# Kernel tuning notes

Hardware: AMD Instinct MI355X
Metric: run time of the kernel (lower is better)

## Reference

```python
import jax, jax.numpy as jnp
import numpy as np

N_NODES = 10000
N_EDGES = 160000
HIDDEN = 64
NUM_RBF = 32
Q_DIM = 8
CUTOFF_UPPER = 5.0


def silu(x):
    return x * jax.nn.sigmoid(x)


def tensor_norm(X):
    # X: [n, 3, 3, H] -> [n, H] (Frobenius norm squared over the 3x3 dims)
    return (X * X).sum(axis=(1, 2))


def decompose_tensor(X):
    # X: [n, 3, 3, H] -> I: [n, H] (trace/3), A: antisym [n,3,3,H], S: sym traceless [n,3,3,H]
    eye = jnp.eye(3, dtype=X.dtype)[None, :, :, None]
    I = jnp.einsum('naah->nh', X) / 3.0
    Xt = X.transpose(0, 2, 1, 3)
    A = 0.5 * (X - Xt)
    S = 0.5 * (X + Xt) - I[:, None, None, :] * eye
    return I, A, S


def compose_tensor(I, A, S):
    eye = jnp.eye(3, dtype=A.dtype)[None, :, :, None]
    return I[:, None, None, :] * eye + A + S


def tmm(P, Q):
    # 3x3 matmul per (atom, channel): [n,3,3,H] x [n,3,3,H] -> [n,3,3,H]
    return jnp.einsum('nach,ncbh->nabh', P, Q)


def setup_inputs() -> dict:
    key = jax.random.key(0)
    ks = jax.random.split(key, 16)
    H = HIDDEN
    inp = {
        'X': jax.random.normal(ks[0], (N_NODES, 3, 3, H), jnp.float32),
        'charges': jax.random.normal(ks[1], (N_NODES, Q_DIM), jnp.float32),
        'edge_weight': jax.random.uniform(ks[2], (N_EDGES,), jnp.float32) * CUTOFF_UPPER,
        'edge_attr': jax.random.normal(ks[3], (N_EDGES, NUM_RBF), jnp.float32),
        'edge_index': jax.random.randint(ks[4], (2, N_EDGES), 0, N_NODES, jnp.int32),
    }
    d_in = NUM_RBF + 2 * Q_DIM
    inp['Ws1'] = jax.random.normal(ks[5], (d_in, H), jnp.float32) / np.sqrt(d_in).astype(np.float32)
    inp['bs1'] = jnp.zeros((H,), jnp.float32)
    inp['Ws2'] = jax.random.normal(ks[6], (H, 2 * H), jnp.float32) / np.sqrt(H).astype(np.float32)
    inp['bs2'] = jnp.zeros((2 * H,), jnp.float32)
    inp['Ws3'] = jax.random.normal(ks[7], (2 * H, 3 * H), jnp.float32) / np.sqrt(2 * H).astype(np.float32)
    inp['bs3'] = jnp.zeros((3 * H,), jnp.float32)
    for i in range(6):
        inp['Wt%d' % i] = jax.random.normal(ks[8 + i], (H, H), jnp.float32) / np.sqrt(H).astype(np.float32)
    return inp


def reference(X, charges, edge_weight, edge_attr, Ws1, bs1, Ws2, bs2, Ws3, bs3,
              Wt0, Wt1, Wt2, Wt3, Wt4, Wt5, edge_index):
    H = HIDDEN
    n = X.shape[0]
    row, col = edge_index[0], edge_index[1]
    # cosine cutoff (cutoff_lower = 0)
    C = 0.5 * (jnp.cos(edge_weight * (jnp.pi / CUTOFF_UPPER)) + 1.0)
    C = C * (edge_weight < CUTOFF_UPPER).astype(X.dtype)
    # edge scalar MLP on [rbf, q_i, q_j]
    h = jnp.concatenate([edge_attr, charges[row], charges[col]], axis=-1)
    h = silu(h @ Ws1 + bs1)
    h = silu(h @ Ws2 + bs2)
    h = silu(h @ Ws3 + bs3)
    w = (h * C[:, None]).reshape(h.shape[0], 3, H)  # [E, 3, H]
    # normalize node tensors
    X = X / (tensor_norm(X) + 1.0)[:, None, None, :]
    I, A, S = decompose_tensor(X)
    I = I @ Wt0
    A = A @ Wt1
    S = S @ Wt2
    Y = compose_tensor(I, A, S)
    # message passing: gather I/A/S at source (edge_index[1]), weight per component, scatter-add at dest (edge_index[0])
    eye = jnp.eye(3, dtype=X.dtype)[None, :, :, None]
    msg_e = ((w[:, 0] * I[col])[:, None, None, :] * eye
             + w[:, 1][:, None, None, :] * A[col]
             + w[:, 2][:, None, None, :] * S[col])  # [E, 3, 3, H]
    msg = jax.ops.segment_sum(msg_e, row, num_segments=n)  # [n, 3, 3, H]
    # O(3): C = msg @ Y + Y @ msg (3x3 matmul per channel)
    Cm = tmm(msg, Y) + tmm(Y, msg)
    I2, A2, S2 = decompose_tensor(Cm)
    normp1 = tensor_norm(Cm) + 1.0
    I2 = I2 / normp1
    A2 = A2 / normp1[:, None, None, :]
    S2 = S2 / normp1[:, None, None, :]
    I2 = I2 @ Wt3
    A2 = A2 @ Wt4
    S2 = S2 @ Wt5
    dX = compose_tensor(I2, A2, S2)
    return X + dX + tmm(dX, dX)
```

## Files before the change

### kernel.cpp

```cpp
#include <hip/hip_runtime.h>
#include <math.h>

#define HD 64

typedef _Float16 half8 __attribute__((ext_vector_type(8)));
typedef _Float16 half4v __attribute__((ext_vector_type(4)));
typedef float floatx4 __attribute__((ext_vector_type(4)));

__device__ __forceinline__ float silu_f(float x) {
    return x * __builtin_amdgcn_rcpf(1.0f + __expf(-x));
}

__global__ __launch_bounds__(256) void node_pre(
    const float* __restrict__ X,
    const float* __restrict__ Wt0, const float* __restrict__ Wt1, const float* __restrict__ Wt2,
    float* __restrict__ Tn, _Float16* __restrict__ TnH, int N)
{
    int sub = threadIdx.x >> 6;
    int h = threadIdx.x & 63;
    int n = blockIdx.x * 4 + sub;
    int nn = (n < N) ? n : (N - 1);

    const float* Xb = X + (size_t)nn * 9 * HD + h;
    float x[9];
    float nrm = 0.f;
#pragma unroll
    for (int i = 0; i < 9; ++i) { x[i] = Xb[i * HD]; nrm += x[i] * x[i]; }
    float inv = 1.0f / (nrm + 1.0f);
#pragma unroll
    for (int i = 0; i < 9; ++i) x[i] *= inv;

    float I0 = (x[0] + x[4] + x[8]) * (1.0f / 3.0f);
    __shared__ float comp[4][10][HD];
    comp[sub][0][h] = I0;
    comp[sub][1][h] = 0.5f * (x[1] - x[3]);
    comp[sub][2][h] = 0.5f * (x[2] - x[6]);
    comp[sub][3][h] = 0.5f * (x[5] - x[7]);
    comp[sub][4][h] = x[0] - I0;
    comp[sub][5][h] = 0.5f * (x[1] + x[3]);
    comp[sub][6][h] = 0.5f * (x[2] + x[6]);
    comp[sub][7][h] = x[4] - I0;
    comp[sub][8][h] = 0.5f * (x[5] + x[7]);
    comp[sub][9][h] = x[8] - I0;
    __syncthreads();
    float acc[10];
#pragma unroll
    for (int i = 0; i < 10; ++i) acc[i] = 0.f;
    for (int k = 0; k < HD; ++k) {
        float w0 = Wt0[k * HD + h];
        float w1 = Wt1[k * HD + h];
        float w2 = Wt2[k * HD + h];
        acc[0] += comp[sub][0][k] * w0;
        acc[1] += comp[sub][1][k] * w1;
        acc[2] += comp[sub][2][k] * w1;
        acc[3] += comp[sub][3][k] * w1;
#pragma unroll
        for (int j = 0; j < 6; ++j) acc[4 + j] += comp[sub][4 + j][k] * w2;
    }
    if (n < N) {
        float* tp = Tn + (size_t)n * 640 + h;
        _Float16* th = TnH + (size_t)n * 640 + h;
#pragma unroll
        for (int i = 0; i < 10; ++i) {
            tp[i * 64] = acc[i];
            th[i * 64] = (_Float16)acc[i];
        }
    }
}

__global__ __launch_bounds__(256) void count_kernel(
    const int* __restrict__ edge_index, int* __restrict__ cnt, int E)
{
    int e = blockIdx.x * 256 + threadIdx.x;
    if (e < E) atomicAdd(&cnt[edge_index[e]], 1);
}

__global__ __launch_bounds__(1024) void scanA(
    const int* __restrict__ cnt, int* __restrict__ offs, int* __restrict__ partial, int N)
{
    __shared__ int wsum[16];
    int tid = threadIdx.x, wid = tid >> 6, lane = tid & 63;
    int i = blockIdx.x * 1024 + tid;
    int v = (i < N) ? cnt[i] : 0;
    int s = v;
#pragma unroll
    for (int d = 1; d < 64; d <<= 1) {
        int t = __shfl_up(s, d, 64);
        if (lane >= d) s += t;
    }
    if (lane == 63) wsum[wid] = s;
    __syncthreads();
    if (tid == 0) {
        int run = 0;
#pragma unroll
        for (int w = 0; w < 16; ++w) { int t = wsum[w]; wsum[w] = run; run += t; }
        partial[blockIdx.x] = run;
    }
    __syncthreads();
    if (i < N) offs[i] = wsum[wid] + s - v;
}

__global__ __launch_bounds__(64) void scanB(int* __restrict__ partial, int nb)
{
    int lane = threadIdx.x;
    int v = (lane < nb) ? partial[lane] : 0;
    int s = v;
#pragma unroll
    for (int d = 1; d < 64; d <<= 1) {
        int t = __shfl_up(s, d, 64);
        if (lane >= d) s += t;
    }
    if (lane < nb) partial[lane] = s - v;
}

__global__ __launch_bounds__(256) void scanC(
    int* __restrict__ offs, const int* __restrict__ partial, int* __restrict__ curs,
    int N, int E)
{
    int i = blockIdx.x * 256 + threadIdx.x;
    if (i < N) {
        int o = offs[i] + partial[i >> 10];
        offs[i] = o;
        curs[i] = o;
    }
    if (i == 0) offs[N] = E;
}

__global__ __launch_bounds__(256) void place_kernel(
    const int* __restrict__ edge_index, int* __restrict__ curs,
    int* __restrict__ rank, int* __restrict__ colP, int E)
{
    int e = blockIdx.x * 256 + threadIdx.x;
    if (e < E) {
        int p = atomicAdd(&curs[edge_index[e]], 1);
        rank[e] = p;
        colP[p] = edge_index[E + e];
    }
}

__global__ __launch_bounds__(256) void wconv(
    const float* __restrict__ Ws1, const float* __restrict__ Ws2, const float* __restrict__ Ws3,
    _Float16* __restrict__ W1f, _Float16* __restrict__ W2f, _Float16* __restrict__ W3f)
{
    int id = blockIdx.x * 256 + threadIdx.x;
    if (id < 4096) {
        int i = id & 7, l = (id >> 3) & 63, t = id >> 9;
        int s = t >> 2, nt = t & 3;
        int k = s * 32 + (l >> 4) * 8 + i;
        int n = nt * 16 + (l & 15);
        W1f[id] = (k < 48) ? (_Float16)Ws1[k * 64 + n] : (_Float16)0.f;
    } else if (id < 4096 + 8192) {
        int j = id - 4096;
        int i = j & 7, l = (j >> 3) & 63, t = j >> 9;
        int s = t >> 3, nt = t & 7;
        int k = s * 32 + (l >> 4) * 8 + i;
        int n = nt * 16 + (l & 15);
        W2f[j] = (_Float16)Ws2[k * 128 + n];
    } else if (id < 4096 + 8192 + 24576) {
        int j = id - 4096 - 8192;
        int i = j & 7, l = (j >> 3) & 63, t = j >> 9;
        int s = t / 12, nt = t % 12;
        int k = s * 32 + (l >> 4) * 8 + i;
        int n = nt * 16 + (l & 15);
        W3f[j] = (_Float16)Ws3[k * 192 + n];
    }
}

__global__ __launch_bounds__(256, 4) void mlp_mfma(
    const float* __restrict__ edge_attr, const float* __restrict__ charges,
    const float* __restrict__ edge_weight, const int* __restrict__ edge_index,
    const int* __restrict__ rank,
    const _Float16* __restrict__ W1f, const float* __restrict__ bs1,
    const _Float16* __restrict__ W2f, const float* __restrict__ bs2,
    const _Float16* __restrict__ W3f, const float* __restrict__ bs3,
    _Float16* __restrict__ bufH, int E)
{
    __shared__ __align__(16) _Float16 act[4][16][200];
    __shared__ float cvsS[4][16];
    __shared__ int rankSS[4][16];

    int tid = threadIdx.x;
    int wv = tid >> 6, l = tid & 63;
    int base = blockIdx.x * 64 + wv * 16;
    int row16 = l & 15, quad = l >> 4;

#pragma unroll
    for (int i = 0; i < 4; ++i) {
        int slot = l + i * 64;
        int e_l = slot >> 4, f = slot & 15;
        int e = base + e_l;
        int ee = (e < E) ? e : (E - 1);
        float4 v = make_float4(0.f, 0.f, 0.f, 0.f);
        if (f < 8) {
            v = *(const float4*)(edge_attr + (size_t)ee * 32 + f * 4);
        } else if (f < 10) {
            int r = edge_index[ee];
            v = *(const float4*)(charges + (size_t)r * 8 + (f - 8) * 4);
        } else if (f < 12) {
            int c = edge_index[E + ee];
            v = *(const float4*)(charges + (size_t)c * 8 + (f - 10) * 4);
        }
        half4v hv = { (_Float16)v.x, (_Float16)v.y, (_Float16)v.z, (_Float16)v.w };
        *(half4v*)&act[wv][e_l][f * 4] = hv;
    }
    if (l < 16) {
        int e = base + l;
        int ee = (e < E) ? e : (E - 1);
        rankSS[wv][l] = rank[ee];
        float wgt = edge_weight[ee];
        float cv = 0.5f * (__cosf(wgt * 0.6283185307179586f) + 1.0f);
        cvsS[wv][l] = (wgt < 5.0f) ? cv : 0.0f;
    }

    half8 A[4];
    A[0] = *(const half8*)&act[wv][row16][quad * 8];
    A[1] = *(const half8*)&act[wv][row16][32 + quad * 8];
    floatx4 acc1[4];
    {
        half8 W[8];
#pragma unroll
        for (int t = 0; t < 8; ++t)
            W[t] = *(const half8*)(W1f + ((size_t)t * 64 + l) * 8);
#pragma unroll
        for (int nt = 0; nt < 4; ++nt) {
            floatx4 c = {0.f, 0.f, 0.f, 0.f};
            c = __builtin_amdgcn_mfma_f32_16x16x32_f16(A[0], W[nt], c, 0, 0, 0);
            c = __builtin_amdgcn_mfma_f32_16x16x32_f16(A[1], W[4 + nt], c, 0, 0, 0);
            acc1[nt] = c;
        }
    }
#pragma unroll
    for (int nt = 0; nt < 4; ++nt) {
        float b = bs1[nt * 16 + row16];
#pragma unroll
        for (int r = 0; r < 4; ++r)
            act[wv][quad * 4 + r][64 + nt * 16 + row16] = (_Float16)silu_f(acc1[nt][r] + b);
    }

    A[0] = *(const half8*)&act[wv][row16][64 + quad * 8];
    A[1] = *(const half8*)&act[wv][row16][96 + quad * 8];
    floatx4 acc2[8];
#pragma unroll
    for (int nt = 0; nt < 8; ++nt) acc2[nt] = (floatx4){0.f, 0.f, 0.f, 0.f};
#pragma unroll
    for (int s = 0; s < 2; ++s) {
        half8 W[8];
#pragma unroll
        for (int nt = 0; nt < 8; ++nt)
            W[nt] = *(const half8*)(W2f + ((size_t)(s * 8 + nt) * 64 + l) * 8);
#pragma unroll
        for (int nt = 0; nt < 8; ++nt)
            acc2[nt] = __builtin_amdgcn_mfma_f32_16x16x32_f16(A[s], W[nt], acc2[nt], 0, 0, 0);
    }
#pragma unroll
    for (int nt = 0; nt < 8; ++nt) {
        float b = bs2[nt * 16 + row16];
#pragma unroll
        for (int r = 0; r < 4; ++r)
            act[wv][quad * 4 + r][nt * 16 + row16] = (_Float16)silu_f(acc2[nt][r] + b);
    }

    A[0] = *(const half8*)&act[wv][row16][quad * 8];
    A[1] = *(const half8*)&act[wv][row16][32 + quad * 8];
    A[2] = *(const half8*)&act[wv][row16][64 + quad * 8];
    A[3] = *(const half8*)&act[wv][row16][96 + quad * 8];

    float cvrow[4];
#pragma unroll
    for (int r = 0; r < 4; ++r) cvrow[r] = cvsS[wv][quad * 4 + r];

#pragma unroll
    for (int g = 0; g < 2; ++g) {
        floatx4 acc3[6];
#pragma unroll
        for (int j = 0; j < 6; ++j) acc3[j] = (floatx4){0.f, 0.f, 0.f, 0.f};
#pragma unroll
        for (int s = 0; s < 4; ++s) {
            half8 W[6];
#pragma unroll
            for (int j = 0; j < 6; ++j)
                W[j] = *(const half8*)(W3f + ((size_t)(s * 12 + g * 6 + j) * 64 + l) * 8);
#pragma unroll
            for (int j = 0; j < 6; ++j)
                acc3[j] = __builtin_amdgcn_mfma_f32_16x16x32_f16(A[s], W[j], acc3[j], 0, 0, 0);
        }
#pragma unroll
        for (int j = 0; j < 6; ++j) {
            int nt = g * 6 + j;
            float b = bs3[nt * 16 + row16];
#pragma unroll
            for (int r = 0; r < 4; ++r)
                act[wv][quad * 4 + r][nt * 16 + row16] =
                    (_Float16)(silu_f(acc3[j][r] + b) * cvrow[r]);
        }
    }
    {
        int fr = l >> 2;
        int ef = base + fr;
        if (ef < E) {
            _Float16* dst = bufH + (size_t)rankSS[wv][fr] * 192;
#pragma unroll
            for (int i = 0; i < 6; ++i) {
                int j = (l & 3) + i * 4;
                *(half8*)(dst + j * 8) = *(const half8*)&act[wv][fr][j * 8];
            }
        }
    }
}

__global__ __launch_bounds__(256) void msg_kernel(
    const _Float16* __restrict__ bufH, const int* __restrict__ colP,
    const int* __restrict__ offs, const _Float16* __restrict__ TnH,
    float* __restrict__ Mn, int N)
{
    __shared__ float part[2][2][10][64];
    int slot = threadIdx.x >> 7;
    int half = (threadIdx.x >> 6) & 1;
    int lane = threadIdx.x & 63;
    int n = blockIdx.x * 2 + slot;
    int nn = (n < N) ? n : (N - 1);
    int beg = offs[nn], end = offs[nn + 1];
    int mid = beg + ((end - beg + 1) >> 1);
    int s0 = half ? mid : beg;
    int s1 = half ? end : mid;

    float a0 = 0.f, a1 = 0.f, a2 = 0.f, a3 = 0.f, a4 = 0.f;
    float a5 = 0.f, a6 = 0.f, a7 = 0.f, a8 = 0.f, a9 = 0.f;
#pragma unroll 2
    for (int idx = s0; idx < s1; ++idx) {
        int c = colP[idx];
        const _Float16* wp = bufH + (size_t)idx * 192;
        float w0 = (float)wp[lane];
        float w1 = (float)wp[64 + lane];
        float w2 = (float)wp[128 + lane];
        const _Float16* tp = TnH + (size_t)c * 640;
        a0 += w0 * (float)tp[lane];
        a1 += w1 * (float)tp[64 + lane];
        a2 += w1 * (float)tp[128 + lane];
        a3 += w1 * (float)tp[192 + lane];
        a4 += w2 * (float)tp[256 + lane];
        a5 += w2 * (float)tp[320 + lane];
        a6 += w2 * (float)tp[384 + lane];
        a7 += w2 * (float)tp[448 + lane];
        a8 += w2 * (float)tp[512 + lane];
        a9 += w2 * (float)tp[576 + lane];
    }
    part[slot][half][0][lane] = a0; part[slot][half][1][lane] = a1;
    part[slot][half][2][lane] = a2; part[slot][half][3][lane] = a3;
    part[slot][half][4][lane] = a4; part[slot][half][5][lane] = a5;
    part[slot][half][6][lane] = a6; part[slot][half][7][lane] = a7;
    part[slot][half][8][lane] = a8; part[slot][half][9][lane] = a9;
    __syncthreads();

    if (n < N) {
        float* mp = Mn + (size_t)n * 640;
#pragma unroll
        for (int j = 0; j < 5; ++j) {
            int c = half * 5 + j;
            mp[c * 64 + lane] = part[slot][0][c][lane] + part[slot][1][c][lane];
        }
    }
}

__global__ __launch_bounds__(256) void node_post(
    const float* __restrict__ X,
    const float* __restrict__ Tn, const float* __restrict__ Mn,
    const float* __restrict__ Wt3, const float* __restrict__ Wt4, const float* __restrict__ Wt5,
    float* __restrict__ out, int N)
{
    int sub = threadIdx.x >> 6;
    int h = threadIdx.x & 63;
    int n = blockIdx.x * 4 + sub;
    int nn = (n < N) ? n : (N - 1);

    const float* Xb = X + (size_t)nn * 9 * HD + h;
    float x[9];
    float nr = 0.f;
#pragma unroll
    for (int i = 0; i < 9; ++i) { x[i] = Xb[i * HD]; nr += x[i] * x[i]; }
    float xinv = 1.0f / (nr + 1.0f);
#pragma unroll
    for (int i = 0; i < 9; ++i) x[i] *= xinv;

    const float* tp = Tn + (size_t)nn * 640 + h;
    const float* mp = Mn + (size_t)nn * 640 + h;
    float yI = tp[0], mI = mp[0];
    float yA[3], yS[6], mA[3], mS[6];
#pragma unroll
    for (int j = 0; j < 3; ++j) { yA[j] = tp[(1 + j) * 64]; mA[j] = mp[(1 + j) * 64]; }
#pragma unroll
    for (int j = 0; j < 6; ++j) { yS[j] = tp[(4 + j) * 64]; mS[j] = mp[(4 + j) * 64]; }

    float M[3][3] = {
        { mI + mS[0],     mA[0] + mS[1],   mA[1] + mS[2] },
        { -mA[0] + mS[1], mI + mS[3],      mA[2] + mS[4] },
        { -mA[1] + mS[2], -mA[2] + mS[4],  mI + mS[5] } };
    float Y[3][3] = {
        { yI + yS[0],     yA[0] + yS[1],   yA[1] + yS[2] },
        { -yA[0] + yS[1], yI + yS[3],      yA[2] + yS[4] },
        { -yA[1] + yS[2], -yA[2] + yS[4],  yI + yS[5] } };

    float Cm[3][3];
    float nrm = 0.f;
#pragma unroll
    for (int a = 0; a < 3; ++a) {
#pragma unroll
        for (int b = 0; b < 3; ++b) {
            float s = 0.f;
#pragma unroll
            for (int c = 0; c < 3; ++c) s += M[a][c] * Y[c][b] + Y[a][c] * M[c][b];
            Cm[a][b] = s;
            nrm += s * s;
        }
    }
    float inv = 1.0f / (nrm + 1.0f);
    float tr3 = (Cm[0][0] + Cm[1][1] + Cm[2][2]) * (1.0f / 3.0f);

    __shared__ float comp[4][10][HD];
    comp[sub][0][h] = tr3 * inv;
    comp[sub][1][h] = 0.5f * (Cm[0][1] - Cm[1][0]) * inv;
    comp[sub][2][h] = 0.5f * (Cm[0][2] - Cm[2][0]) * inv;
    comp[sub][3][h] = 0.5f * (Cm[1][2] - Cm[2][1]) * inv;
    comp[sub][4][h] = (Cm[0][0] - tr3) * inv;
    comp[sub][5][h] = 0.5f * (Cm[0][1] + Cm[1][0]) * inv;
    comp[sub][6][h] = 0.5f * (Cm[0][2] + Cm[2][0]) * inv;
    comp[sub][7][h] = (Cm[1][1] - tr3) * inv;
    comp[sub][8][h] = 0.5f * (Cm[1][2] + Cm[2][1]) * inv;
    comp[sub][9][h] = (Cm[2][2] - tr3) * inv;
    __syncthreads();

    float acc[10];
#pragma unroll
    for (int i = 0; i < 10; ++i) acc[i] = 0.f;
    for (int k = 0; k < HD; ++k) {
        float w3 = Wt3[k * HD + h];
        float w4 = Wt4[k * HD + h];
        float w5 = Wt5[k * HD + h];
        acc[0] += comp[sub][0][k] * w3;
        acc[1] += comp[sub][1][k] * w4;
        acc[2] += comp[sub][2][k] * w4;
        acc[3] += comp[sub][3][k] * w4;
#pragma unroll
        for (int j = 0; j < 6; ++j) acc[4 + j] += comp[sub][4 + j][k] * w5;
    }
    float D[3][3] = {
        { acc[0] + acc[4],  acc[1] + acc[5],  acc[2] + acc[6] },
        { -acc[1] + acc[5], acc[0] + acc[7],  acc[3] + acc[8] },
        { -acc[2] + acc[6], -acc[3] + acc[8], acc[0] + acc[9] } };

    if (n < N) {
        float* ob = out + (size_t)n * 9 * HD + h;
#pragma unroll
        for (int a = 0; a < 3; ++a) {
#pragma unroll
            for (int b = 0; b < 3; ++b) {
                float s = 0.f;
#pragma unroll
                for (int c = 0; c < 3; ++c) s += D[a][c] * D[c][b];
                ob[(a * 3 + b) * HD] = x[a * 3 + b] + D[a][b] + s;
            }
        }
    }
}

extern "C" void kernel_launch(void* const* d_in, const int* in_sizes, int n_in,
                              void* d_out, int out_size, void* d_ws, size_t ws_size,
                              hipStream_t stream)
{
    const float* X           = (const float*)d_in[0];
    const float* charges     = (const float*)d_in[1];
    const float* edge_weight = (const float*)d_in[2];
    const float* edge_attr   = (const float*)d_in[3];
    const int*   edge_index  = (const int*)d_in[4];
    const float* Ws1 = (const float*)d_in[5];
    const float* bs1 = (const float*)d_in[6];
    const float* Ws2 = (const float*)d_in[7];
    const float* bs2 = (const float*)d_in[8];
    const float* Ws3 = (const float*)d_in[9];
    const float* bs3 = (const float*)d_in[10];
    const float* Wt0 = (const float*)d_in[11];
    const float* Wt1 = (const float*)d_in[12];
    const float* Wt2 = (const float*)d_in[13];
    const float* Wt3 = (const float*)d_in[14];
    const float* Wt4 = (const float*)d_in[15];
    const float* Wt5 = (const float*)d_in[16];

    int N = in_sizes[0] / (9 * HD);
    int E = in_sizes[2];

    float* ws = (float*)d_ws;
    float* Tn  = ws;
    float* Mn  = Tn + (size_t)N * 640;
    _Float16* TnH  = (_Float16*)(Mn + (size_t)N * 640);
    _Float16* bufH = TnH + (size_t)N * 640;
    int* cnt   = (int*)(bufH + (size_t)E * 192);
    int* offs  = cnt + N;
    int* curs  = offs + N + 1;
    int* rank  = curs + N;
    int* colP  = rank + E;
    int* partial = colP + E;
    size_t fofs = ((size_t)((char*)(partial + 64) - (char*)d_ws) + 15) & ~(size_t)15;
    _Float16* W1f = (_Float16*)((char*)d_ws + fofs);
    _Float16* W2f = W1f + 4096;
    _Float16* W3f = W2f + 8192;

    hipMemsetAsync(cnt, 0, (size_t)N * sizeof(int), stream);

    int nbE256 = (E + 255) / 256;
    int nbN1024 = (N + 1023) / 1024;
    count_kernel<<<nbE256, 256, 0, stream>>>(edge_index, cnt, E);
    scanA<<<nbN1024, 1024, 0, stream>>>(cnt, offs, partial, N);
    scanB<<<1, 64, 0, stream>>>(partial, nbN1024);
    scanC<<<(N + 255) / 256, 256, 0, stream>>>(offs, partial, curs, N, E);
    place_kernel<<<nbE256, 256, 0, stream>>>(edge_index, curs, rank, colP, E);

    wconv<<<144, 256, 0, stream>>>(Ws1, Ws2, Ws3, W1f, W2f, W3f);

    node_pre<<<(N + 3) / 4, 256, 0, stream>>>(X, Wt0, Wt1, Wt2, Tn, TnH, N);

    int nbE64 = (E + 63) / 64;
    mlp_mfma<<<nbE64, 256, 0, stream>>>(edge_attr, charges, edge_weight, edge_index,
                                        rank, W1f, bs1, W2f, bs2, W3f, bs3, bufH, E);

    msg_kernel<<<(N + 1) / 2, 256, 0, stream>>>(bufH, colP, offs, TnH, Mn, N);

    node_post<<<(N + 3) / 4, 256, 0, stream>>>(X, Tn, Mn, Wt3, Wt4, Wt5, (float*)d_out, N);
}
```

Before: 178.8 us.

## Merge small kernels and give each MLP wave two 16-edge tiles

The weight-conversion kernel is folded into node_pre as extra blocks of one launch, and the single-block scanB is removed by having scanC sum the preceding block partials itself. mlp_mfma now runs 128-thread blocks in which each wave handles 32 edges as two M-tiles, so every loaded weight fragment feeds two MFMAs. This cuts launch count and weight-load traffic per edge. The cost is more accumulator registers per wave and a per-thread serial loop over partials in scanC.

```diff
diff --git a/kernel.cpp b/kernel.cpp
--- a/kernel.cpp
+++ b/kernel.cpp
@@ -11,11 +11,39 @@
     return x * __builtin_amdgcn_rcpf(1.0f + __expf(-x));
 }
 
-__global__ __launch_bounds__(256) void node_pre(
+__global__ __launch_bounds__(256) void pre_wconv(
     const float* __restrict__ X,
     const float* __restrict__ Wt0, const float* __restrict__ Wt1, const float* __restrict__ Wt2,
-    float* __restrict__ Tn, _Float16* __restrict__ TnH, int N)
-{
+    float* __restrict__ Tn, _Float16* __restrict__ TnH, int N, int nbPre,
+    const float* __restrict__ Ws1, const float* __restrict__ Ws2, const float* __restrict__ Ws3,
+    _Float16* __restrict__ W1f, _Float16* __restrict__ W2f, _Float16* __restrict__ W3f)
+{
+    if (blockIdx.x >= nbPre) {
+        int id = (blockIdx.x - nbPre) * 256 + threadIdx.x;
+        if (id < 4096) {
+            int i = id & 7, l = (id >> 3) & 63, t = id >> 9;
+            int s = t >> 2, nt = t & 3;
+            int k = s * 32 + (l >> 4) * 8 + i;
+            int n = nt * 16 + (l & 15);
+            W1f[id] = (k < 48) ? (_Float16)Ws1[k * 64 + n] : (_Float16)0.f;
+        } else if (id < 4096 + 8192) {
+            int j = id - 4096;
+            int i = j & 7, l = (j >> 3) & 63, t = j >> 9;
+            int s = t >> 3, nt = t & 7;
+            int k = s * 32 + (l >> 4) * 8 + i;
+            int n = nt * 16 + (l & 15);
+            W2f[j] = (_Float16)Ws2[k * 128 + n];
+        } else if (id < 4096 + 8192 + 24576) {
+            int j = id - 4096 - 8192;
+            int i = j & 7, l = (j >> 3) & 63, t = j >> 9;
+            int s = t / 12, nt = t % 12;
+            int k = s * 32 + (l >> 4) * 8 + i;
+            int n = nt * 16 + (l & 15);
+            W3f[j] = (_Float16)Ws3[k * 192 + n];
+        }
+        return;
+    }
+
     int sub = threadIdx.x >> 6;
     int h = threadIdx.x & 63;
     int n = blockIdx.x * 4 + sub;
@@ -100,26 +128,16 @@
     if (i < N) offs[i] = wsum[wid] + s - v;
 }
 
-__global__ __launch_bounds__(64) void scanB(int* __restrict__ partial, int nb)
-{
-    int lane = threadIdx.x;
-    int v = (lane < nb) ? partial[lane] : 0;
-    int s = v;
-#pragma unroll
-    for (int d = 1; d < 64; d <<= 1) {
-        int t = __shfl_up(s, d, 64);
-        if (lane >= d) s += t;
-    }
-    if (lane < nb) partial[lane] = s - v;
-}
-
 __global__ __launch_bounds__(256) void scanC(
     int* __restrict__ offs, const int* __restrict__ partial, int* __restrict__ curs,
     int N, int E)
 {
     int i = blockIdx.x * 256 + threadIdx.x;
     if (i < N) {
-        int o = offs[i] + partial[i >> 10];
+        int b = i >> 10;
+        int basev = 0;
+        for (int w = 0; w < b; ++w) basev += partial[w];
+        int o = offs[i] + basev;
         offs[i] = o;
         curs[i] = o;
     }
@@ -138,35 +156,7 @@
     }
 }
 
-__global__ __launch_bounds__(256) void wconv(
-    const float* __restrict__ Ws1, const float* __restrict__ Ws2, const float* __restrict__ Ws3,
-    _Float16* __restrict__ W1f, _Float16* __restrict__ W2f, _Float16* __restrict__ W3f)
-{
-    int id = blockIdx.x * 256 + threadIdx.x;
-    if (id < 4096) {
-        int i = id & 7, l = (id >> 3) & 63, t = id >> 9;
-        int s = t >> 2, nt = t & 3;
-        int k = s * 32 + (l >> 4) * 8 + i;
-        int n = nt * 16 + (l & 15);
-        W1f[id] = (k < 48) ? (_Float16)Ws1[k * 64 + n] : (_Float16)0.f;
-    } else if (id < 4096 + 8192) {
-        int j = id - 4096;
-        int i = j & 7, l = (j >> 3) & 63, t = j >> 9;
-        int s = t >> 3, nt = t & 7;
-        int k = s * 32 + (l >> 4) * 8 + i;
-        int n = nt * 16 + (l & 15);
-        W2f[j] = (_Float16)Ws2[k * 128 + n];
-    } else if (id < 4096 + 8192 + 24576) {
-        int j = id - 4096 - 8192;
-        int i = j & 7, l = (j >> 3) & 63, t = j >> 9;
-        int s = t / 12, nt = t % 12;
-        int k = s * 32 + (l >> 4) * 8 + i;
-        int n = nt * 16 + (l & 15);
-        W3f[j] = (_Float16)Ws3[k * 192 + n];
-    }
-}
-
-__global__ __launch_bounds__(256, 4) void mlp_mfma(
+__global__ __launch_bounds__(128, 4) void mlp_mfma(
     const float* __restrict__ edge_attr, const float* __restrict__ charges,
     const float* __restrict__ edge_weight, const int* __restrict__ edge_index,
     const int* __restrict__ rank,
@@ -175,17 +165,17 @@
     const _Float16* __restrict__ W3f, const float* __restrict__ bs3,
     _Float16* __restrict__ bufH, int E)
 {
-    __shared__ __align__(16) _Float16 act[4][16][200];
-    __shared__ float cvsS[4][16];
-    __shared__ int rankSS[4][16];
+    __shared__ __align__(16) _Float16 act[2][32][200];
+    __shared__ float cvsS[2][32];
+    __shared__ int rankSS[2][32];
 
     int tid = threadIdx.x;
     int wv = tid >> 6, l = tid & 63;
-    int base = blockIdx.x * 64 + wv * 16;
+    int base = blockIdx.x * 64 + wv * 32;
     int row16 = l & 15, quad = l >> 4;
 
 #pragma unroll
-    for (int i = 0; i < 4; ++i) {
+    for (int i = 0; i < 8; ++i) {
         int slot = l + i * 64;
         int e_l = slot >> 4, f = slot & 15;
         int e = base + e_l;
@@ -203,7 +193,7 @@
         half4v hv = { (_Float16)v.x, (_Float16)v.y, (_Float16)v.z, (_Float16)v.w };
         *(half4v*)&act[wv][e_l][f * 4] = hv;
     }
-    if (l < 16) {
+    if (l < 32) {
         int e = base + l;
         int ee = (e < E) ? e : (E - 1);
         rankSS[wv][l] = rank[ee];
@@ -212,90 +202,127 @@
         cvsS[wv][l] = (wgt < 5.0f) ? cv : 0.0f;
     }
 
-    half8 A[4];
-    A[0] = *(const half8*)&act[wv][row16][quad * 8];
-    A[1] = *(const half8*)&act[wv][row16][32 + quad * 8];
-    floatx4 acc1[4];
+    half8 A[2][2];
+#pragma unroll
+    for (int m = 0; m < 2; ++m) {
+        A[m][0] = *(const half8*)&act[wv][m * 16 + row16][quad * 8];
+        A[m][1] = *(const half8*)&act[wv][m * 16 + row16][32 + quad * 8];
+    }
     {
         half8 W[8];
 #pragma unroll
         for (int t = 0; t < 8; ++t)
             W[t] = *(const half8*)(W1f + ((size_t)t * 64 + l) * 8);
+        floatx4 acc[2][4];
+#pragma unroll
+        for (int nt = 0; nt < 4; ++nt)
+#pragma unroll
+            for (int m = 0; m < 2; ++m) {
+                floatx4 c = {0.f, 0.f, 0.f, 0.f};
+                c = __builtin_amdgcn_mfma_f32_16x16x32_f16(A[m][0], W[nt], c, 0, 0, 0);
+                c = __builtin_amdgcn_mfma_f32_16x16x32_f16(A[m][1], W[4 + nt], c, 0, 0, 0);
+                acc[m][nt] = c;
+            }
 #pragma unroll
         for (int nt = 0; nt < 4; ++nt) {
-            floatx4 c = {0.f, 0.f, 0.f, 0.f};
-            c = __builtin_amdgcn_mfma_f32_16x16x32_f16(A[0], W[nt], c, 0, 0, 0);
-            c = __builtin_amdgcn_mfma_f32_16x16x32_f16(A[1], W[4 + nt], c, 0, 0, 0);
-            acc1[nt] = c;
-        }
-    }
-#pragma unroll
-    for (int nt = 0; nt < 4; ++nt) {
-        float b = bs1[nt * 16 + row16];
-#pragma unroll
-        for (int r = 0; r < 4; ++r)
-            act[wv][quad * 4 + r][64 + nt * 16 + row16] = (_Float16)silu_f(acc1[nt][r] + b);
-    }
-
-    A[0] = *(const half8*)&act[wv][row16][64 + quad * 8];
-    A[1] = *(const half8*)&act[wv][row16][96 + quad * 8];
-    floatx4 acc2[8];
-#pragma unroll
-    for (int nt = 0; nt < 8; ++nt) acc2[nt] = (floatx4){0.f, 0.f, 0.f, 0.f};
-#pragma unroll
-    for (int s = 0; s < 2; ++s) {
+            float b = bs1[nt * 16 + row16];
+#pragma unroll
+            for (int m = 0; m < 2; ++m)
+#pragma unroll
+                for (int r = 0; r < 4; ++r)
+                    act[wv][m * 16 + quad * 4 + r][64 + nt * 16 + row16] =
+                        (_Float16)silu_f(acc[m][nt][r] + b);
+        }
+    }
+
+#pragma unroll
+    for (int m = 0; m < 2; ++m) {
+        A[m][0] = *(const half8*)&act[wv][m * 16 + row16][64 + quad * 8];
+        A[m][1] = *(const half8*)&act[wv][m * 16 + row16][96 + quad * 8];
+    }
+#pragma unroll
+    for (int g = 0; g < 2; ++g) {
         half8 W[8];
 #pragma unroll
-        for (int nt = 0; nt < 8; ++nt)
-            W[nt] = *(const half8*)(W2f + ((size_t)(s * 8 + nt) * 64 + l) * 8);
-#pragma unroll
-        for (int nt = 0; nt < 8; ++nt)
-            acc2[nt] = __builtin_amdgcn_mfma_f32_16x16x32_f16(A[s], W[nt], acc2[nt], 0, 0, 0);
-    }
-#pragma unroll
-    for (int nt = 0; nt < 8; ++nt) {
-        float b = bs2[nt * 16 + row16];
-#pragma unroll
-        for (int r = 0; r < 4; ++r)
-            act[wv][quad * 4 + r][nt * 16 + row16] = (_Float16)silu_f(acc2[nt][r] + b);
-    }
-
-    A[0] = *(const half8*)&act[wv][row16][quad * 8];
-    A[1] = *(const half8*)&act[wv][row16][32 + quad * 8];
-    A[2] = *(const half8*)&act[wv][row16][64 + quad * 8];
-    A[3] = *(const half8*)&act[wv][row16][96 + quad * 8];
-
-    float cvrow[4];
-#pragma unroll
-    for (int r = 0; r < 4; ++r) cvrow[r] = cvsS[wv][quad * 4 + r];
-
-#pragma unroll
-    for (int g = 0; g < 2; ++g) {
-        floatx4 acc3[6];
-#pragma unroll
-        for (int j = 0; j < 6; ++j) acc3[j] = (floatx4){0.f, 0.f, 0.f, 0.f};
+        for (int s = 0; s < 2; ++s)
+#pragma unroll
+            for (int j = 0; j < 4; ++j)
+                W[s * 4 + j] = *(const half8*)(W2f + ((size_t)(s * 8 + g * 4 + j) * 64 + l) * 8);
+        floatx4 acc[2][4];
+#pragma unroll
+        for (int m = 0; m < 2; ++m)
+#pragma unroll
+            for (int j = 0; j < 4; ++j) acc[m][j] = (floatx4){0.f, 0.f, 0.f, 0.f};
+#pragma unroll
+        for (int s = 0; s < 2; ++s)
+#pragma unroll
+            for (int j = 0; j < 4; ++j)
+#pragma unroll
+                for (int m = 0; m < 2; ++m)
+                    acc[m][j] = __builtin_amdgcn_mfma_f32_16x16x32_f16(
+                                    A[m][s], W[s * 4 + j], acc[m][j], 0, 0, 0);
+#pragma unroll
+        for (int j = 0; j < 4; ++j) {
+            int nt = g * 4 + j;
+            float b = bs2[nt * 16 + row16];
+#pragma unroll
+            for (int m = 0; m < 2; ++m)
+#pragma unroll
+                for (int r = 0; r < 4; ++r)
+                    act[wv][m * 16 + quad * 4 + r][nt * 16 + row16] =
+                        (_Float16)silu_f(acc[m][j][r] + b);
+        }
+    }
+
+    half8 A3[2][4];
+#pragma unroll
+    for (int m = 0; m < 2; ++m)
+#pragma unroll
+        for (int s = 0; s < 4; ++s)
+            A3[m][s] = *(const half8*)&act[wv][m * 16 + row16][s * 32 + quad * 8];
+
+    float cvrow[2][4];
+#pragma unroll
+    for (int m = 0; m < 2; ++m)
+#pragma unroll
+        for (int r = 0; r < 4; ++r) cvrow[m][r] = cvsS[wv][m * 16 + quad * 4 + r];
+
+#pragma unroll
+    for (int g = 0; g < 3; ++g) {
+        floatx4 acc[2][4];
+#pragma unroll
+        for (int m = 0; m < 2; ++m)
+#pragma unroll
+            for (int j = 0; j < 4; ++j) acc[m][j] = (floatx4){0.f, 0.f, 0.f, 0.f};
 #pragma unroll
         for (int s = 0; s < 4; ++s) {
-            half8 W[6];
-#pragma unroll
-            for (int j = 0; j < 6; ++j)
-                W[j] = *(const half8*)(W3f + ((size_t)(s * 12 + g * 6 + j) * 64 + l) * 8);
-#pragma unroll
-            for (int j = 0; j < 6; ++j)
-                acc3[j] = __builtin_amdgcn_mfma_f32_16x16x32_f16(A[s], W[j], acc3[j], 0, 0, 0);
-        }
-#pragma unroll
-        for (int j = 0; j < 6; ++j) {
-            int nt = g * 6 + j;
+            half8 W[4];
+#pragma unroll
+            for (int j = 0; j < 4; ++j)
+                W[j] = *(const half8*)(W3f + ((size_t)(s * 12 + g * 4 + j) * 64 + l) * 8);
+#pragma unroll
+            for (int j = 0; j < 4; ++j)
+#pragma unroll
+                for (int m = 0; m < 2; ++m)
+                    acc[m][j] = __builtin_amdgcn_mfma_f32_16x16x32_f16(
+                                    A3[m][s], W[j], acc[m][j], 0, 0, 0);
+        }
+#pragma unroll
+        for (int j = 0; j < 4; ++j) {
+            int nt = g * 4 + j;
             float b = bs3[nt * 16 + row16];
 #pragma unroll
-            for (int r = 0; r < 4; ++r)
-                act[wv][quad * 4 + r][nt * 16 + row16] =
-                    (_Float16)(silu_f(acc3[j][r] + b) * cvrow[r]);
-        }
-    }
-    {
-        int fr = l >> 2;
+            for (int m = 0; m < 2; ++m)
+#pragma unroll
+                for (int r = 0; r < 4; ++r)
+                    act[wv][m * 16 + quad * 4 + r][nt * 16 + row16] =
+                        (_Float16)(silu_f(acc[m][j][r] + b) * cvrow[m][r]);
+        }
+    }
+
+#pragma unroll
+    for (int p = 0; p < 2; ++p) {
+        int fr = (l >> 2) + p * 16;
         int ef = base + fr;
         if (ef < E) {
             _Float16* dst = bufH + (size_t)rankSS[wv][fr] * 192;
@@ -510,16 +537,15 @@
     int nbN1024 = (N + 1023) / 1024;
     count_kernel<<<nbE256, 256, 0, stream>>>(edge_index, cnt, E);
     scanA<<<nbN1024, 1024, 0, stream>>>(cnt, offs, partial, N);
-    scanB<<<1, 64, 0, stream>>>(partial, nbN1024);
     scanC<<<(N + 255) / 256, 256, 0, stream>>>(offs, partial, curs, N, E);
     place_kernel<<<nbE256, 256, 0, stream>>>(edge_index, curs, rank, colP, E);
 
-    wconv<<<144, 256, 0, stream>>>(Ws1, Ws2, Ws3, W1f, W2f, W3f);
-
-    node_pre<<<(N + 3) / 4, 256, 0, stream>>>(X, Wt0, Wt1, Wt2, Tn, TnH, N);
+    int nbPre = (N + 3) / 4;
+    pre_wconv<<<nbPre + 144, 256, 0, stream>>>(X, Wt0, Wt1, Wt2, Tn, TnH, N, nbPre,
+                                               Ws1, Ws2, Ws3, W1f, W2f, W3f);
 
     int nbE64 = (E + 63) / 64;
-    mlp_mfma<<<nbE64, 256, 0, stream>>>(edge_attr, charges, edge_weight, edge_index,
+    mlp_mfma<<<nbE64, 128, 0, stream>>>(edge_attr, charges, edge_weight, edge_index,
                                         rank, W1f, bs1, W2f, bs2, W3f, bs3, bufH, E);
 
     msg_kernel<<<(N + 1) / 2, 256, 0, stream>>>(bufH, colP, offs, TnH, Mn, N);
```

Result: slower. 187.2 us (+4.7%).
